# Kernel tuning notes

Hardware: AMD Instinct MI355X
Metric: run time of the kernel (lower is better)

## Reference

```python
import jax, jax.numpy as jnp
import numpy as np

B, T, E, H = 2, 2048, 1024, 16
D = E // H  # head_dim = 64


def setup_inputs() -> dict:
    key = jax.random.key(0)
    kx, kq, kk, kv, ko = jax.random.split(key, 5)
    x = jax.random.normal(kx, (B, T, E), dtype=jnp.float32)
    # nn.Parameter(torch.randn(...)) -> standard normal params
    Wq = jax.random.normal(kq, (H, E, D), dtype=jnp.float32)
    Wk = jax.random.normal(kk, (H, E, D), dtype=jnp.float32)
    Wv = jax.random.normal(kv, (H, E, D), dtype=jnp.float32)
    # nn.Linear(E, E, bias=False): weight [out, in], y = a @ Wo.T
    Wo = jax.random.normal(ko, (E, E), dtype=jnp.float32) * (1.0 / np.sqrt(E))
    # boolean mask: True positions are filled with -inf (causal: strict upper tri)
    mask = jnp.triu(jnp.ones((T, T), dtype=bool), k=1)
    return {"x": x, "mask": mask, "Wq": Wq, "Wk": Wk, "Wv": Wv, "Wo": Wo}


def reference(x, mask, Wq, Wk, Wv, Wo):
    # x: [b, t, e]; Wq/Wk/Wv: [h, e, i]
    q = jnp.einsum('hei,bte->hbti', Wq, x)
    k = jnp.einsum('hei,bte->hbti', Wk, x)
    v = jnp.einsum('hei,bte->hbti', Wv, x)
    # NOTE: original scales by sqrt(seq_len) (x.shape[1]), not sqrt(head_dim)
    scale = x.shape[1] ** 0.5
    fit = jnp.einsum('hbti,hbTi->hbtT', q, k) / scale  # [h, b, t, T]
    fit = jnp.where(mask, -jnp.inf, fit)
    p = jax.nn.softmax(fit, axis=-1)
    att = jnp.einsum('hbtT,hbTi->hbti', p, v)          # [h, b, t, i]
    # rearrange 'h b t i -> b t (h i)'
    b, t = att.shape[1], att.shape[2]
    att = jnp.transpose(att, (1, 2, 0, 3)).reshape(b, t, -1)
    return att @ Wo.T
```

## Files before the change

kernel.cpp:

```cpp
#include <hip/hip_runtime.h>
#include <hip/hip_fp8.h>
#include <stdint.h>

constexpr float INV_SCALE = 0.022097086912079608f;
constexpr float LOG2E = 1.4426950408889634f;
constexpr float QSC = INV_SCALE * LOG2E;

typedef __attribute__((ext_vector_type(8))) short bfrag;
typedef __attribute__((ext_vector_type(4))) float facc;
typedef __attribute__((ext_vector_type(4))) unsigned short us4;

#define MFMA(a, b, c) __builtin_amdgcn_mfma_f32_16x16x32_bf16((a), (b), (c), 0, 0, 0)
#define EXP2(x) __builtin_amdgcn_exp2f(x)

__device__ __forceinline__ unsigned short f2bh(float f) {
    union { float f; unsigned int u; } cv; cv.f = f;
    unsigned int u = cv.u;
    u += 0x7FFFu + ((u >> 16) & 1u);
    return (unsigned short)(u >> 16);
}
__device__ __forceinline__ float bh2f(unsigned short h) {
    union { unsigned int u; float f; } cv; cv.u = ((unsigned int)h) << 16;
    return cv.f;
}
__device__ __forceinline__ void gl_lds16(const unsigned short* g, unsigned short* lds) {
    __builtin_amdgcn_global_load_lds(
        (const __attribute__((address_space(1))) unsigned int*)g,
        (__attribute__((address_space(3))) unsigned int*)lds, 16, 0, 0);
}
__device__ __forceinline__ bfrag f8frag(uint2 raw) {
    union { uint2 u; unsigned char b[8]; } cv; cv.u = raw;
    bfrag r;
    #pragma unroll
    for (int j = 0; j < 8; ++j) {
        const __hip_fp8_e4m3* t = reinterpret_cast<const __hip_fp8_e4m3*>(&cv.b[j]);
        r[j] = (short)f2bh((float)(*t) * 0.00390625f);
    }
    return r;
}
template<int CTRL>
__device__ __forceinline__ float dppmax(float v) {
    int s = __builtin_amdgcn_update_dpp(0, __builtin_bit_cast(int, v), CTRL, 0xF, 0xF, true);
    return fmaxf(v, __builtin_bit_cast(float, s));
}
__device__ __forceinline__ float rowmax16(float v) {
    v = dppmax<0xB1>(v);
    v = dppmax<0x4E>(v);
    v = dppmax<0x141>(v);
    v = dppmax<0x140>(v);
    return v;
}

__global__ __launch_bounds__(256) void prep_xw(const float* __restrict__ x,
                                               const float* __restrict__ Wo,
                                               unsigned short* __restrict__ xh,
                                               unsigned short* __restrict__ xl,
                                               unsigned short* __restrict__ WoB) {
    if (blockIdx.x < 1024) {
        int idx = blockIdx.x * 256 + threadIdx.x;
        facc v = *(const facc*)&Wo[(size_t)idx * 4];
        us4 o;
        #pragma unroll
        for (int j = 0; j < 4; ++j) o[j] = f2bh(v[j]);
        *(us4*)&WoB[(size_t)idx * 4] = o;
    } else {
        int idx = (blockIdx.x - 1024) * 256 + threadIdx.x;
        facc v = *(const facc*)&x[(size_t)idx * 4];
        us4 hv, lv;
        #pragma unroll
        for (int j = 0; j < 4; ++j) {
            unsigned short hb = f2bh(v[j]);
            hv[j] = hb;
            lv[j] = f2bh(v[j] - bh2f(hb));
        }
        *(us4*)&xh[(size_t)idx * 4] = hv;
        *(us4*)&xl[(size_t)idx * 4] = lv;
    }
}

__global__ __launch_bounds__(256) void prep_w(
    const float* __restrict__ Wq, const float* __restrict__ Wk, const float* __restrict__ Wv,
    unsigned short* __restrict__ WqTh, unsigned short* __restrict__ WqTl,
    unsigned short* __restrict__ WkTh, unsigned short* __restrict__ WkTl,
    unsigned short* __restrict__ WvT)
{
    __shared__ float tile[64][65];
    const int tid = threadIdx.x;
    const int et = blockIdx.x, h = blockIdx.y, m = blockIdx.z;
    const float* W = (m == 0) ? Wq : (m == 1) ? Wk : Wv;
    #pragma unroll
    for (int rep = 0; rep < 4; ++rep) {
        int idx = rep * 256 + tid;
        int e = idx >> 4, i4 = (idx & 15) * 4;
        facc v = *(const facc*)&W[(size_t)h * 65536 + (size_t)(et * 64 + e) * 64 + i4];
        tile[e][i4] = v.x; tile[e][i4 + 1] = v.y; tile[e][i4 + 2] = v.z; tile[e][i4 + 3] = v.w;
    }
    __syncthreads();
    unsigned short* Oh = (m == 0) ? WqTh : (m == 1) ? WkTh : WvT;
    unsigned short* Ol = (m == 0) ? WqTl : WkTl;
    #pragma unroll
    for (int rep = 0; rep < 4; ++rep) {
        int idx = rep * 256 + tid;
        int i = idx >> 4, e4 = (idx & 15) * 4;
        us4 hv, lv;
        #pragma unroll
        for (int j = 0; j < 4; ++j) {
            float f = tile[e4 + j][i];
            unsigned short hb = f2bh(f);
            hv[j] = hb;
            lv[j] = f2bh(f - bh2f(hb));
        }
        size_t o = (size_t)(h * 64 + i) * 1024 + et * 64 + e4;
        *(us4*)&Oh[o] = hv;
        if (m < 2) *(us4*)&Ol[o] = lv;
    }
}

__global__ __launch_bounds__(256, 2) void qkv_fused(
    const unsigned short* __restrict__ xh, const unsigned short* __restrict__ xl,
    const unsigned short* __restrict__ WqTh, const unsigned short* __restrict__ WqTl,
    const unsigned short* __restrict__ WkTh, const unsigned short* __restrict__ WkTl,
    const unsigned short* __restrict__ WvT,
    unsigned short* __restrict__ qh, unsigned char* __restrict__ ql8,
    unsigned short* __restrict__ kh, unsigned short* __restrict__ kl,
    unsigned short* __restrict__ vT)
{
    extern __shared__ unsigned short sm[];
    unsigned short* Ab = sm;
    unsigned short* Qb = sm + 16384;
    unsigned short* Kb = sm + 24576;
    unsigned short* Vb = sm + 32768;
    const int tid = threadIdx.x;
    const int w = tid >> 6, l = tid & 63;
    const int wm = w >> 1, wn = w & 1;
    const int ct = blockIdx.x, rt = blockIdx.y;

    const int lc = (l & 7) ^ (l >> 3);
    const int krel = (lc & 3) * 8;
    const unsigned short* Axp = (lc < 4) ? xh : xl;
    const unsigned short* Qp  = (lc < 4) ? WqTh : WqTl;
    const unsigned short* Kp  = (lc < 4) ? WkTh : WkTl;
    const int lcv = (l & 3) ^ ((l >> 3) & 3);

    facc accq[4][2], acck[4][2], accv[4][2];
    #pragma unroll
    for (int m = 0; m < 4; ++m)
        #pragma unroll
        for (int n = 0; n < 2; ++n) {
            accq[m][n] = (facc)(0.0f); acck[m][n] = (facc)(0.0f); accv[m][n] = (facc)(0.0f);
        }

    auto stageV = [&](int buf, int e0) {
        int row = w * 16 + (l >> 2);
        gl_lds16(&WvT[(size_t)(ct * 64 + row) * 1024 + e0 + lcv * 8],
                 &Vb[buf * 2048 + w * 512]);
    };

    {
        #pragma unroll
        for (int i = 0; i < 4; ++i) {
            int slice = w * 4 + i;
            int row = slice * 8 + (l >> 3);
            gl_lds16(&Axp[(size_t)(rt * 128 + row) * 1024 + krel], &Ab[slice * 512]);
        }
        #pragma unroll
        for (int i = 0; i < 2; ++i) {
            int slice = w * 2 + i;
            int row = slice * 8 + (l >> 3);
            size_t sb = (size_t)(ct * 64 + row) * 1024 + krel;
            gl_lds16(&Qp[sb], &Qb[slice * 512]);
            gl_lds16(&Kp[sb], &Kb[slice * 512]);
        }
        stageV(0, 0);
    }
    asm volatile("s_waitcnt vmcnt(0)" ::: "memory");
    __builtin_amdgcn_s_barrier();

    for (int t = 0; t < 32; ++t) {
        __builtin_amdgcn_s_barrier();
        __builtin_amdgcn_sched_barrier(0);
        if (t < 31) {
            int buf = (t + 1) & 1, e0 = (t + 1) * 32;
            #pragma unroll
            for (int i = 0; i < 4; ++i) {
                int slice = w * 4 + i;
                int row = slice * 8 + (l >> 3);
                gl_lds16(&Axp[(size_t)(rt * 128 + row) * 1024 + e0 + krel],
                         &Ab[buf * 8192 + slice * 512]);
            }
            #pragma unroll
            for (int i = 0; i < 2; ++i) {
                int slice = w * 2 + i;
                int row = slice * 8 + (l >> 3);
                size_t sb = (size_t)(ct * 64 + row) * 1024 + e0 + krel;
                gl_lds16(&Qp[sb], &Qb[buf * 4096 + slice * 512]);
                gl_lds16(&Kp[sb], &Kb[buf * 4096 + slice * 512]);
            }
            stageV(buf, e0);
        }
        __builtin_amdgcn_sched_barrier(0);
        if (t < 31) asm volatile("s_waitcnt vmcnt(9)" ::: "memory");
        else        asm volatile("s_waitcnt vmcnt(0)" ::: "memory");
        __builtin_amdgcn_sched_barrier(0);
        __builtin_amdgcn_s_barrier();
        __builtin_amdgcn_sched_barrier(0);

        const unsigned short* Ac = &Ab[(t & 1) * 8192];
        const unsigned short* Qc = &Qb[(t & 1) * 4096];
        const unsigned short* Kc = &Kb[(t & 1) * 4096];
        const unsigned short* Vc = &Vb[(t & 1) * 2048];
        const int ca = (l >> 4) ^ (l & 7);
        const int cb = ca ^ 4;

        bfrag afh[4], afl[4];
        #pragma unroll
        for (int m = 0; m < 4; ++m) {
            int row = wm * 64 + m * 16 + (l & 15);
            afh[m] = *(const bfrag*)&Ac[row * 64 + ca * 8];
            afl[m] = *(const bfrag*)&Ac[row * 64 + cb * 8];
        }
        #pragma unroll
        for (int n = 0; n < 2; ++n) {
            int nr = wn * 32 + n * 16 + (l & 15);
            int cv = (l >> 4) ^ ((nr >> 1) & 3);
            bfrag bv = *(const bfrag*)&Vc[nr * 32 + cv * 8];
            #pragma unroll
            for (int m = 0; m < 4; ++m) accv[m][n] = MFMA(afh[m], bv, accv[m][n]);
        }
        #pragma unroll
        for (int n = 0; n < 2; ++n) {
            int nr = wn * 32 + n * 16 + (l & 15);
            bfrag bh = *(const bfrag*)&Qc[nr * 64 + ca * 8];
            bfrag bl = *(const bfrag*)&Qc[nr * 64 + cb * 8];
            #pragma unroll
            for (int m = 0; m < 4; ++m) {
                accq[m][n] = MFMA(afh[m], bh, accq[m][n]);
                accq[m][n] = MFMA(afh[m], bl, accq[m][n]);
                accq[m][n] = MFMA(afl[m], bh, accq[m][n]);
            }
        }
        #pragma unroll
        for (int n = 0; n < 2; ++n) {
            int nr = wn * 32 + n * 16 + (l & 15);
            bfrag bh = *(const bfrag*)&Kc[nr * 64 + ca * 8];
            bfrag bl = *(const bfrag*)&Kc[nr * 64 + cb * 8];
            #pragma unroll
            for (int m = 0; m < 4; ++m) {
                acck[m][n] = MFMA(afh[m], bh, acck[m][n]);
                acck[m][n] = MFMA(afh[m], bl, acck[m][n]);
                acck[m][n] = MFMA(afl[m], bh, acck[m][n]);
            }
        }
    }

    #pragma unroll
    for (int m = 0; m < 4; ++m)
        #pragma unroll
        for (int r = 0; r < 4; ++r) {
            int row = rt * 128 + wm * 64 + m * 16 + (l >> 4) * 4 + r;
            #pragma unroll
            for (int n = 0; n < 2; ++n) {
                int col = ct * 64 + wn * 32 + n * 16 + (l & 15);
                float fq = accq[m][n][r] * QSC;
                unsigned short hb = f2bh(fq);
                qh[(size_t)row * 1024 + col] = hb;
                __hip_fp8_e4m3 e((fq - bh2f(hb)) * 256.0f);
                ql8[(size_t)row * 1024 + col] = *reinterpret_cast<unsigned char*>(&e);
                float fk = acck[m][n][r];
                unsigned short kb = f2bh(fk);
                kh[(size_t)row * 1024 + col] = kb;
                kl[(size_t)row * 1024 + col] = f2bh(fk - bh2f(kb));
            }
        }
    #pragma unroll
    for (int m = 0; m < 4; ++m) {
        int t0g = rt * 128 + wm * 64 + m * 16 + (l >> 4) * 4;
        int b_ = t0g >> 11, t0 = t0g & 2047;
        #pragma unroll
        for (int n = 0; n < 2; ++n) {
            int col = ct * 64 + wn * 32 + n * 16 + (l & 15);
            int h_ = col >> 6, d = col & 63;
            us4 pk;
            #pragma unroll
            for (int r = 0; r < 4; ++r) pk[r] = f2bh(accv[m][n][r]);
            *(us4*)&vT[((size_t)((h_ * 2 + b_) * 64 + d)) * 2048 + t0] = pk;
        }
    }
}

__device__ __forceinline__ void stage_k(
    const unsigned short* __restrict__ kh, const unsigned short* __restrict__ kl,
    unsigned short* Khb, unsigned short* Klb, int w, int l, int b, int h, int kt)
{
    #pragma unroll
    for (int i = 0; i < 2; ++i) {
        int pbase = (w * 2 + i) * 1024;
        int p = pbase + l * 16;
        int row = p >> 7, slot = (p >> 4) & 7;
        int chunk = slot ^ (row & 7);
        size_t srcK = (size_t)(b * 2048 + kt * 64 + row) * 1024 + h * 64 + chunk * 8;
        gl_lds16(&kh[srcK], &Khb[pbase >> 1]);
        gl_lds16(&kl[srcK], &Klb[pbase >> 1]);
    }
}
__device__ __forceinline__ void stage_v(
    const unsigned short* __restrict__ vT, unsigned short* Vtb,
    int w, int l, int b, int h, int kt)
{
    #pragma unroll
    for (int i = 0; i < 2; ++i) {
        int pbase = (w * 2 + i) * 1024;
        int p = pbase + l * 16;
        int row = p >> 7, slot = (p >> 4) & 7;
        int chunk = slot ^ (row & 7);
        size_t srcV = ((size_t)(h * 2 + b) * 64 + row) * 2048 + (size_t)kt * 64 + chunk * 8;
        gl_lds16(&vT[srcV], &Vtb[pbase >> 1]);
    }
}

__global__ __launch_bounds__(256, 3) void attn_mfma(
    const unsigned short* __restrict__ qh, const unsigned char* __restrict__ ql8,
    const unsigned short* __restrict__ kh, const unsigned short* __restrict__ kl,
    const unsigned short* __restrict__ vT, unsigned short* __restrict__ att)
{
    __shared__ unsigned short Kh[2][4096], Kl[2][4096], Vt[4096], Pl[4096];
    const int tid = threadIdx.x, w = tid >> 6, l = tid & 63;
    const int dd = blockIdx.y * 32 + blockIdx.x;
    const int xcd = dd & 7, sl = dd >> 3;
    const int qt = 31 - (sl >> 2);
    const int hb = xcd * 4 + (sl & 3);
    const int h = hb >> 1, b = hb & 1;

    bfrag ones;
    #pragma unroll
    for (int j = 0; j < 8; ++j) ones[j] = (short)0x3F80;

    bfrag qfh[2], qfl[2];
    {
        const int qrow = qt * 64 + w * 16 + (l & 15);
        const size_t qoff = (size_t)(b * 2048 + qrow) * 1024 + h * 64 + (l >> 4) * 8;
        qfh[0] = *(const bfrag*)&qh[qoff];
        qfh[1] = *(const bfrag*)&qh[qoff + 32];
        qfl[0] = f8frag(*(const uint2*)&ql8[qoff]);
        qfl[1] = f8frag(*(const uint2*)&ql8[qoff + 32]);
    }

    facc O[4], Osum;
    float mrow[4];
    #pragma unroll
    for (int f = 0; f < 4; ++f) O[f] = (facc)(0.0f);
    Osum = (facc)(0.0f);
    #pragma unroll
    for (int r = 0; r < 4; ++r) mrow[r] = -1e30f;

    stage_k(kh, kl, Kh[0], Kl[0], w, l, b, h, 0);
    for (int kt = 0; kt <= qt; ++kt) {
        const int cur = kt & 1;
        __syncthreads();
        stage_v(vT, Vt, w, l, b, h, kt);
        if (kt < qt)
            stage_k(kh, kl, Kh[cur ^ 1], Kl[cur ^ 1], w, l, b, h, kt + 1);
        __builtin_amdgcn_sched_barrier(0);
        __builtin_amdgcn_s_barrier();
        __builtin_amdgcn_sched_barrier(0);

        facc S[4];
        #pragma unroll
        for (int f = 0; f < 4; ++f) S[f] = (facc)(0.0f);
        __builtin_amdgcn_s_setprio(1);
        #pragma unroll
        for (int s = 0; s < 2; ++s) {
            #pragma unroll
            for (int f = 0; f < 4; ++f) {
                int key = f * 16 + (l & 15);
                int ch = (s * 4 + (l >> 4)) ^ (key & 7);
                bfrag kbh = *(const bfrag*)&Kh[cur][key * 64 + ch * 8];
                bfrag kbl = *(const bfrag*)&Kl[cur][key * 64 + ch * 8];
                S[f] = MFMA(qfh[s], kbh, S[f]);
                S[f] = MFMA(qfh[s], kbl, S[f]);
                S[f] = MFMA(qfl[s], kbh, S[f]);
            }
        }
        __builtin_amdgcn_s_setprio(0);
        if (kt == qt) {
            #pragma unroll
            for (int f = 0; f < 4; ++f) {
                int keyl = f * 16 + (l & 15);
                #pragma unroll
                for (int r = 0; r < 4; ++r) {
                    int qls = w * 16 + (l >> 4) * 4 + r;
                    if (keyl > qls) S[f][r] = -1e30f;
                }
            }
        }
        float mx[4];
        float dmax = -3.0e38f;
        #pragma unroll
        for (int r = 0; r < 4; ++r) {
            float m0 = fmaxf(fmaxf(S[0][r], S[1][r]), fmaxf(S[2][r], S[3][r]));
            m0 = rowmax16(m0);
            mx[r] = m0;
            dmax = fmaxf(dmax, m0 - mrow[r]);
        }
        if (!__all(dmax <= 8.0f)) {
            #pragma unroll
            for (int r = 0; r < 4; ++r) {
                float mn = fmaxf(mrow[r], mx[r]);
                float fac = EXP2(mrow[r] - mn);
                mrow[r] = mn;
                O[0][r] *= fac; O[1][r] *= fac; O[2][r] *= fac; O[3][r] *= fac;
                Osum[r] *= fac;
            }
        }
        #pragma unroll
        for (int r = 0; r < 4; ++r)
            #pragma unroll
            for (int f = 0; f < 4; ++f) S[f][r] = EXP2(S[f][r] - mrow[r]);
        #pragma unroll
        for (int f = 0; f < 4; ++f) {
            int key = f * 16 + (l & 15);
            #pragma unroll
            for (int r = 0; r < 4; ++r) {
                int qr = w * 16 + (l >> 4) * 4 + r;
                Pl[qr * 64 + (((key >> 3) ^ (qr & 7)) * 8) + (key & 7)] = f2bh(S[f][r]);
            }
        }
        __builtin_amdgcn_sched_barrier(0);
        if (kt < qt) asm volatile("s_waitcnt vmcnt(4)" ::: "memory");
        else         asm volatile("s_waitcnt vmcnt(0)" ::: "memory");
        __builtin_amdgcn_sched_barrier(0);
        __builtin_amdgcn_s_barrier();
        __builtin_amdgcn_sched_barrier(0);
        __builtin_amdgcn_s_setprio(1);
        #pragma unroll
        for (int s = 0; s < 2; ++s) {
            int qa = w * 16 + (l & 15);
            int cha = (s * 4 + (l >> 4)) ^ (qa & 7);
            bfrag pa = *(const bfrag*)&Pl[qa * 64 + cha * 8];
            Osum = MFMA(pa, ones, Osum);
            #pragma unroll
            for (int f = 0; f < 4; ++f) {
                int d = f * 16 + (l & 15);
                int chv = (s * 4 + (l >> 4)) ^ (d & 7);
                bfrag vb = *(const bfrag*)&Vt[d * 64 + chv * 8];
                O[f] = MFMA(pa, vb, O[f]);
            }
        }
        __builtin_amdgcn_s_setprio(0);
    }

    #pragma unroll
    for (int f = 0; f < 4; ++f) {
        int d = h * 64 + f * 16 + (l & 15);
        #pragma unroll
        for (int r = 0; r < 4; ++r) {
            int t = qt * 64 + w * 16 + (l >> 4) * 4 + r;
            att[(size_t)(b * 2048 + t) * 1024 + d] = f2bh(O[f][r] / Osum[r]);
        }
    }
}

__global__ __launch_bounds__(256, 2) void outproj(
    const unsigned short* __restrict__ att, const unsigned short* __restrict__ WoB,
    float* __restrict__ out)
{
    __shared__ unsigned short Ab[2][128 * 64], Bb[2][128 * 64];
    const int tid = threadIdx.x, w = tid >> 6, l = tid & 63;
    const int wm = w >> 1, wn = w & 1;
    const int rt = blockIdx.x, ct = blockIdx.y;

    const int lc = (l & 7) ^ (l >> 3);
    facc acc[4][4];
    #pragma unroll
    for (int i = 0; i < 4; ++i)
        #pragma unroll
        for (int j = 0; j < 4; ++j) acc[i][j] = (facc)(0.0f);

    auto stage = [&](int buf, int e0) {
        #pragma unroll
        for (int i = 0; i < 4; ++i) {
            int slice = w * 4 + i;
            int row = slice * 8 + (l >> 3);
            gl_lds16(&att[(size_t)(rt * 128 + row) * 1024 + e0 + lc * 8], &Ab[buf][slice * 512]);
            gl_lds16(&WoB[(size_t)(ct * 128 + row) * 1024 + e0 + lc * 8], &Bb[buf][slice * 512]);
        }
    };

    stage(0, 0);
    int cur = 0;
    for (int t = 0; t < 16; ++t) {
        __syncthreads();
        if (t < 15) stage(cur ^ 1, (t + 1) * 64);
        __builtin_amdgcn_sched_barrier(0);
        __builtin_amdgcn_s_barrier();
        __builtin_amdgcn_sched_barrier(0);
        #pragma unroll
        for (int s = 0; s < 2; ++s) {
            const int slot = (s * 4 + (l >> 4)) ^ (l & 7);
            bfrag af[4], bf_[4];
            #pragma unroll
            for (int m = 0; m < 4; ++m)
                af[m] = *(const bfrag*)&Ab[cur][(wm * 64 + m * 16 + (l & 15)) * 64 + slot * 8];
            #pragma unroll
            for (int n = 0; n < 4; ++n)
                bf_[n] = *(const bfrag*)&Bb[cur][(wn * 64 + n * 16 + (l & 15)) * 64 + slot * 8];
            #pragma unroll
            for (int m = 0; m < 4; ++m)
                #pragma unroll
                for (int n = 0; n < 4; ++n)
                    acc[m][n] = MFMA(af[m], bf_[n], acc[m][n]);
        }
        cur ^= 1;
    }
    #pragma unroll
    for (int m = 0; m < 4; ++m)
        #pragma unroll
        for (int r = 0; r < 4; ++r) {
            int row = rt * 128 + wm * 64 + m * 16 + (l >> 4) * 4 + r;
            #pragma unroll
            for (int n = 0; n < 4; ++n) {
                int col = ct * 128 + wn * 64 + n * 16 + (l & 15);
                out[(size_t)row * 1024 + col] = acc[m][n][r];
            }
        }
}

extern "C" void kernel_launch(void* const* d_in, const int* in_sizes, int n_in,
                              void* d_out, int out_size, void* d_ws, size_t ws_size,
                              hipStream_t stream) {
    const float* x  = (const float*)d_in[0];
    const float* Wq = (const float*)d_in[2];
    const float* Wk = (const float*)d_in[3];
    const float* Wv = (const float*)d_in[4];
    const float* Wo = (const float*)d_in[5];

    uint8_t* wsb = (uint8_t*)d_ws;
    const size_t MB = 1024 * 1024;
    unsigned short* WqTh = (unsigned short*)(wsb + 0 * MB);
    unsigned short* WqTl = (unsigned short*)(wsb + 2 * MB);
    unsigned short* WkTh = (unsigned short*)(wsb + 4 * MB);
    unsigned short* WkTl = (unsigned short*)(wsb + 6 * MB);
    unsigned short* WvT  = (unsigned short*)(wsb + 8 * MB);
    unsigned short* qh   = (unsigned short*)(wsb + 10 * MB);
    unsigned char*  ql8  = (unsigned char*)(wsb + 18 * MB);
    unsigned short* kh   = (unsigned short*)(wsb + 22 * MB);
    unsigned short* kl   = (unsigned short*)(wsb + 30 * MB);
    unsigned short* vT   = (unsigned short*)(wsb + 38 * MB);
    unsigned short* att  = (unsigned short*)(wsb + 46 * MB);
    unsigned short* xh   = (unsigned short*)(wsb + 46 * MB);
    unsigned short* WoB  = (unsigned short*)(wsb + 54 * MB);
    unsigned short* xl   = (unsigned short*)(wsb + 56 * MB);

    hipFuncSetAttribute((const void*)qkv_fused,
                        hipFuncAttributeMaxDynamicSharedMemorySize, 73728);

    prep_xw<<<dim3(5120), 256, 0, stream>>>(x, Wo, xh, xl, WoB);
    prep_w<<<dim3(16, 16, 3), 256, 0, stream>>>(Wq, Wk, Wv, WqTh, WqTl, WkTh, WkTl, WvT);
    qkv_fused<<<dim3(16, 32), 256, 73728, stream>>>(xh, xl, WqTh, WqTl, WkTh, WkTl, WvT,
                                                    qh, ql8, kh, kl, vT);
    attn_mfma<<<dim3(32, 32), 256, 0, stream>>>(qh, ql8, kh, kl, vT, att);
    outproj<<<dim3(32, 8), 256, 0, stream>>>(att, WoB, (float*)d_out);
}
```

Measured before the change: 156.6 us.

## Merge prep kernels, single-buffer K-low tile, raise attention occupancy

The two preprocessing kernels are merged into one launch, removing a kernel launch and its inter-kernel gap. In attention, the K low-part tile moves from double-buffered to single-buffered. Its load is now issued at the top of each iteration and waited on only after the high-part MFMAs, so the S computation is split into two phases with separate vmcnt waits and barriers. The LDS saved allows launch_bounds to go from 3 to 4 blocks per CU. The block-to-tile mapping is also rearranged to alternate causal tile order across slices for load balance, at the cost of one more barrier per iteration and tighter exposure of K-low load latency.

```diff
diff --git a/kernel.cpp b/kernel.cpp
--- a/kernel.cpp
+++ b/kernel.cpp
@@ -51,20 +51,56 @@
     return v;
 }
 
-__global__ __launch_bounds__(256) void prep_xw(const float* __restrict__ x,
-                                               const float* __restrict__ Wo,
-                                               unsigned short* __restrict__ xh,
-                                               unsigned short* __restrict__ xl,
-                                               unsigned short* __restrict__ WoB) {
-    if (blockIdx.x < 1024) {
-        int idx = blockIdx.x * 256 + threadIdx.x;
+__global__ __launch_bounds__(256) void prep_all(
+    const float* __restrict__ x, const float* __restrict__ Wo,
+    const float* __restrict__ Wq, const float* __restrict__ Wk, const float* __restrict__ Wv,
+    unsigned short* __restrict__ xh, unsigned short* __restrict__ xl,
+    unsigned short* __restrict__ WoB,
+    unsigned short* __restrict__ WqTh, unsigned short* __restrict__ WqTl,
+    unsigned short* __restrict__ WkTh, unsigned short* __restrict__ WkTl,
+    unsigned short* __restrict__ WvT)
+{
+    __shared__ float tile[64][65];
+    const int tid = threadIdx.x;
+    const int bx = blockIdx.x;
+    if (bx < 768) {
+        const int et = bx & 15, h = (bx >> 4) & 15, m = bx >> 8;
+        const float* W = (m == 0) ? Wq : (m == 1) ? Wk : Wv;
+        #pragma unroll
+        for (int rep = 0; rep < 4; ++rep) {
+            int idx = rep * 256 + tid;
+            int e = idx >> 4, i4 = (idx & 15) * 4;
+            facc v = *(const facc*)&W[(size_t)h * 65536 + (size_t)(et * 64 + e) * 64 + i4];
+            tile[e][i4] = v.x; tile[e][i4 + 1] = v.y; tile[e][i4 + 2] = v.z; tile[e][i4 + 3] = v.w;
+        }
+        __syncthreads();
+        unsigned short* Oh = (m == 0) ? WqTh : (m == 1) ? WkTh : WvT;
+        unsigned short* Ol = (m == 0) ? WqTl : WkTl;
+        #pragma unroll
+        for (int rep = 0; rep < 4; ++rep) {
+            int idx = rep * 256 + tid;
+            int i = idx >> 4, e4 = (idx & 15) * 4;
+            us4 hv, lv;
+            #pragma unroll
+            for (int j = 0; j < 4; ++j) {
+                float f = tile[e4 + j][i];
+                unsigned short hb = f2bh(f);
+                hv[j] = hb;
+                lv[j] = f2bh(f - bh2f(hb));
+            }
+            size_t o = (size_t)(h * 64 + i) * 1024 + et * 64 + e4;
+            *(us4*)&Oh[o] = hv;
+            if (m < 2) *(us4*)&Ol[o] = lv;
+        }
+    } else if (bx < 1792) {
+        int idx = (bx - 768) * 256 + tid;
         facc v = *(const facc*)&Wo[(size_t)idx * 4];
         us4 o;
         #pragma unroll
         for (int j = 0; j < 4; ++j) o[j] = f2bh(v[j]);
         *(us4*)&WoB[(size_t)idx * 4] = o;
     } else {
-        int idx = (blockIdx.x - 1024) * 256 + threadIdx.x;
+        int idx = (bx - 1792) * 256 + tid;
         facc v = *(const facc*)&x[(size_t)idx * 4];
         us4 hv, lv;
         #pragma unroll
@@ -75,44 +111,6 @@
         }
         *(us4*)&xh[(size_t)idx * 4] = hv;
         *(us4*)&xl[(size_t)idx * 4] = lv;
-    }
-}
-
-__global__ __launch_bounds__(256) void prep_w(
-    const float* __restrict__ Wq, const float* __restrict__ Wk, const float* __restrict__ Wv,
-    unsigned short* __restrict__ WqTh, unsigned short* __restrict__ WqTl,
-    unsigned short* __restrict__ WkTh, unsigned short* __restrict__ WkTl,
-    unsigned short* __restrict__ WvT)
-{
-    __shared__ float tile[64][65];
-    const int tid = threadIdx.x;
-    const int et = blockIdx.x, h = blockIdx.y, m = blockIdx.z;
-    const float* W = (m == 0) ? Wq : (m == 1) ? Wk : Wv;
-    #pragma unroll
-    for (int rep = 0; rep < 4; ++rep) {
-        int idx = rep * 256 + tid;
-        int e = idx >> 4, i4 = (idx & 15) * 4;
-        facc v = *(const facc*)&W[(size_t)h * 65536 + (size_t)(et * 64 + e) * 64 + i4];
-        tile[e][i4] = v.x; tile[e][i4 + 1] = v.y; tile[e][i4 + 2] = v.z; tile[e][i4 + 3] = v.w;
-    }
-    __syncthreads();
-    unsigned short* Oh = (m == 0) ? WqTh : (m == 1) ? WkTh : WvT;
-    unsigned short* Ol = (m == 0) ? WqTl : WkTl;
-    #pragma unroll
-    for (int rep = 0; rep < 4; ++rep) {
-        int idx = rep * 256 + tid;
-        int i = idx >> 4, e4 = (idx & 15) * 4;
-        us4 hv, lv;
-        #pragma unroll
-        for (int j = 0; j < 4; ++j) {
-            float f = tile[e4 + j][i];
-            unsigned short hb = f2bh(f);
-            hv[j] = hb;
-            lv[j] = f2bh(f - bh2f(hb));
-        }
-        size_t o = (size_t)(h * 64 + i) * 1024 + et * 64 + e4;
-        *(us4*)&Oh[o] = hv;
-        if (m < 2) *(us4*)&Ol[o] = lv;
     }
 }
 
@@ -288,9 +286,9 @@
     }
 }
 
-__device__ __forceinline__ void stage_k(
-    const unsigned short* __restrict__ kh, const unsigned short* __restrict__ kl,
-    unsigned short* Khb, unsigned short* Klb, int w, int l, int b, int h, int kt)
+__device__ __forceinline__ void stage_kh(
+    const unsigned short* __restrict__ kh, unsigned short* Khb,
+    int w, int l, int b, int h, int kt)
 {
     #pragma unroll
     for (int i = 0; i < 2; ++i) {
@@ -298,9 +296,22 @@
         int p = pbase + l * 16;
         int row = p >> 7, slot = (p >> 4) & 7;
         int chunk = slot ^ (row & 7);
-        size_t srcK = (size_t)(b * 2048 + kt * 64 + row) * 1024 + h * 64 + chunk * 8;
-        gl_lds16(&kh[srcK], &Khb[pbase >> 1]);
-        gl_lds16(&kl[srcK], &Klb[pbase >> 1]);
+        size_t src = (size_t)(b * 2048 + kt * 64 + row) * 1024 + h * 64 + chunk * 8;
+        gl_lds16(&kh[src], &Khb[pbase >> 1]);
+    }
+}
+__device__ __forceinline__ void stage_kl(
+    const unsigned short* __restrict__ kl, unsigned short* Klb,
+    int w, int l, int b, int h, int kt)
+{
+    #pragma unroll
+    for (int i = 0; i < 2; ++i) {
+        int pbase = (w * 2 + i) * 1024;
+        int p = pbase + l * 16;
+        int row = p >> 7, slot = (p >> 4) & 7;
+        int chunk = slot ^ (row & 7);
+        size_t src = (size_t)(b * 2048 + kt * 64 + row) * 1024 + h * 64 + chunk * 8;
+        gl_lds16(&kl[src], &Klb[pbase >> 1]);
     }
 }
 __device__ __forceinline__ void stage_v(
@@ -318,22 +329,23 @@
     }
 }
 
-__global__ __launch_bounds__(256, 3) void attn_mfma(
+__global__ __launch_bounds__(256, 4) void attn_mfma(
     const unsigned short* __restrict__ qh, const unsigned char* __restrict__ ql8,
     const unsigned short* __restrict__ kh, const unsigned short* __restrict__ kl,
     const unsigned short* __restrict__ vT, unsigned short* __restrict__ att)
 {
-    __shared__ unsigned short Kh[2][4096], Kl[2][4096], Vt[4096], Pl[4096];
+    __shared__ unsigned short Kh[2][4096], Kl[4096], Vt[4096], Pl[4096];
     const int tid = threadIdx.x, w = tid >> 6, l = tid & 63;
     const int dd = blockIdx.y * 32 + blockIdx.x;
-    const int xcd = dd & 7, sl = dd >> 3;
-    const int qt = 31 - (sl >> 2);
-    const int hb = xcd * 4 + (sl & 3);
+    const int s = dd >> 8, c = dd & 255;
+    const int hb = (c & 7) * 4 + s;
+    const int j = c >> 3;
+    const int qt = (s & 1) ? j : 31 - j;
     const int h = hb >> 1, b = hb & 1;
 
     bfrag ones;
     #pragma unroll
-    for (int j = 0; j < 8; ++j) ones[j] = (short)0x3F80;
+    for (int jj = 0; jj < 8; ++jj) ones[jj] = (short)0x3F80;
 
     bfrag qfh[2], qfl[2];
     {
@@ -353,13 +365,18 @@
     #pragma unroll
     for (int r = 0; r < 4; ++r) mrow[r] = -1e30f;
 
-    stage_k(kh, kl, Kh[0], Kl[0], w, l, b, h, 0);
+    stage_kh(kh, Kh[0], w, l, b, h, 0);
     for (int kt = 0; kt <= qt; ++kt) {
         const int cur = kt & 1;
-        __syncthreads();
+        __builtin_amdgcn_s_barrier();
+        __builtin_amdgcn_sched_barrier(0);
+        stage_kl(kl, Kl, w, l, b, h, kt);
         stage_v(vT, Vt, w, l, b, h, kt);
         if (kt < qt)
-            stage_k(kh, kl, Kh[cur ^ 1], Kl[cur ^ 1], w, l, b, h, kt + 1);
+            stage_kh(kh, Kh[cur ^ 1], w, l, b, h, kt + 1);
+        __builtin_amdgcn_sched_barrier(0);
+        if (kt < qt) asm volatile("s_waitcnt vmcnt(6)" ::: "memory");
+        else         asm volatile("s_waitcnt vmcnt(4)" ::: "memory");
         __builtin_amdgcn_sched_barrier(0);
         __builtin_amdgcn_s_barrier();
         __builtin_amdgcn_sched_barrier(0);
@@ -369,16 +386,32 @@
         for (int f = 0; f < 4; ++f) S[f] = (facc)(0.0f);
         __builtin_amdgcn_s_setprio(1);
         #pragma unroll
-        for (int s = 0; s < 2; ++s) {
+        for (int sph = 0; sph < 2; ++sph) {
             #pragma unroll
             for (int f = 0; f < 4; ++f) {
                 int key = f * 16 + (l & 15);
-                int ch = (s * 4 + (l >> 4)) ^ (key & 7);
+                int ch = (sph * 4 + (l >> 4)) ^ (key & 7);
                 bfrag kbh = *(const bfrag*)&Kh[cur][key * 64 + ch * 8];
-                bfrag kbl = *(const bfrag*)&Kl[cur][key * 64 + ch * 8];
-                S[f] = MFMA(qfh[s], kbh, S[f]);
-                S[f] = MFMA(qfh[s], kbl, S[f]);
-                S[f] = MFMA(qfl[s], kbh, S[f]);
+                S[f] = MFMA(qfh[sph], kbh, S[f]);
+                S[f] = MFMA(qfl[sph], kbh, S[f]);
+            }
+        }
+        __builtin_amdgcn_s_setprio(0);
+        __builtin_amdgcn_sched_barrier(0);
+        if (kt < qt) asm volatile("s_waitcnt vmcnt(2)" ::: "memory");
+        else         asm volatile("s_waitcnt vmcnt(0)" ::: "memory");
+        __builtin_amdgcn_sched_barrier(0);
+        __builtin_amdgcn_s_barrier();
+        __builtin_amdgcn_sched_barrier(0);
+        __builtin_amdgcn_s_setprio(1);
+        #pragma unroll
+        for (int sph = 0; sph < 2; ++sph) {
+            #pragma unroll
+            for (int f = 0; f < 4; ++f) {
+                int key = f * 16 + (l & 15);
+                int ch = (sph * 4 + (l >> 4)) ^ (key & 7);
+                bfrag kbl = *(const bfrag*)&Kl[key * 64 + ch * 8];
+                S[f] = MFMA(qfh[sph], kbl, S[f]);
             }
         }
         __builtin_amdgcn_s_setprio(0);
@@ -425,23 +458,17 @@
                 Pl[qr * 64 + (((key >> 3) ^ (qr & 7)) * 8) + (key & 7)] = f2bh(S[f][r]);
             }
         }
-        __builtin_amdgcn_sched_barrier(0);
-        if (kt < qt) asm volatile("s_waitcnt vmcnt(4)" ::: "memory");
-        else         asm volatile("s_waitcnt vmcnt(0)" ::: "memory");
-        __builtin_amdgcn_sched_barrier(0);
-        __builtin_amdgcn_s_barrier();
-        __builtin_amdgcn_sched_barrier(0);
         __builtin_amdgcn_s_setprio(1);
         #pragma unroll
-        for (int s = 0; s < 2; ++s) {
+        for (int sph = 0; sph < 2; ++sph) {
             int qa = w * 16 + (l & 15);
-            int cha = (s * 4 + (l >> 4)) ^ (qa & 7);
+            int cha = (sph * 4 + (l >> 4)) ^ (qa & 7);
             bfrag pa = *(const bfrag*)&Pl[qa * 64 + cha * 8];
             Osum = MFMA(pa, ones, Osum);
             #pragma unroll
             for (int f = 0; f < 4; ++f) {
                 int d = f * 16 + (l & 15);
-                int chv = (s * 4 + (l >> 4)) ^ (d & 7);
+                int chv = (sph * 4 + (l >> 4)) ^ (d & 7);
                 bfrag vb = *(const bfrag*)&Vt[d * 64 + chv * 8];
                 O[f] = MFMA(pa, vb, O[f]);
             }
@@ -554,8 +581,8 @@
     hipFuncSetAttribute((const void*)qkv_fused,
                         hipFuncAttributeMaxDynamicSharedMemorySize, 73728);
 
-    prep_xw<<<dim3(5120), 256, 0, stream>>>(x, Wo, xh, xl, WoB);
-    prep_w<<<dim3(16, 16, 3), 256, 0, stream>>>(Wq, Wk, Wv, WqTh, WqTl, WkTh, WkTl, WvT);
+    prep_all<<<dim3(5888), 256, 0, stream>>>(x, Wo, Wq, Wk, Wv, xh, xl, WoB,
+                                             WqTh, WqTl, WkTh, WkTl, WvT);
     qkv_fused<<<dim3(16, 32), 256, 73728, stream>>>(xh, xl, WqTh, WqTl, WkTh, WkTl, WvT,
                                                     qh, ql8, kh, kl, vT);
     attn_mfma<<<dim3(32, 32), 256, 0, stream>>>(qh, ql8, kh, kl, vT, att);
```

Result: slower. 166.0 us (+6.0%).
